# Kernel tuning notes

Hardware: AMD Instinct MI355X
Metric: run time of the kernel (lower is better)

Reference implementation:

```python
import jax, jax.numpy as jnp
import numpy as np

N = 50000; E = 800000; IN = 256; HID = 128; H = 4; C = 32; L = 3
REL = 100; RD = 16; EH = 32  # rel_emb_dim, edge-encoder hidden
LN_EPS = 1e-5


def _ln(x, g, b):
    m = jnp.mean(x, axis=-1, keepdims=True)
    v = jnp.mean((x - m) ** 2, axis=-1, keepdims=True)
    return (x - m) * jax.lax.rsqrt(v + LN_EPS) * g + b


def _mlp2(x, W1, b1, W2, b2):
    return jax.nn.relu(x @ W1 + b1) @ W2 + b2


def _forward(x, edge_attr, in_g, in_b, proj_W, proj_b,
             dist_W1, dist_b1, dist_W2, dist_b2,
             coexp_W1, coexp_b1, coexp_W2, coexp_b2,
             rel_emb, fus_W1, fus_b1, fus_ln_g, fus_ln_b, fus_W2, fus_b2,
             Wsrc, Wdst, Wedge, att, sscale, ng, nb, edge_index):
    src, dst = edge_index[0], edge_index[1]
    dist_w = edge_attr[:, 0]                              # [E] raw distance weight
    # ---- edge encoder ----
    dist_feat = _mlp2(edge_attr[:, 0:1], dist_W1, dist_b1, dist_W2, dist_b2)   # [E,RD]
    coexp_feat = _mlp2(edge_attr[:, 1:2], coexp_W1, coexp_b1, coexp_W2, coexp_b2)
    rel_id = jnp.clip(edge_attr[:, 2].astype(jnp.int32), 0, REL - 1)
    rel_feat = rel_emb[rel_id]                            # [E,RD]
    comb = jnp.concatenate([dist_feat, coexp_feat, rel_feat], axis=1)          # [E,3*RD]
    h = comb @ fus_W1 + fus_b1
    h = jax.nn.relu(_ln(h, fus_ln_g, fus_ln_b))
    edge_feat = h @ fus_W2 + fus_b2                       # [E,RD]
    # ---- input norm + projection ----
    x = _ln(x, in_g, in_b) @ proj_W + proj_b              # [N,HID]
    # ---- GAT layers ----
    for i in range(L):
        x_res = x
        xs = (x @ Wsrc[i]).reshape(N, H, C)
        xd = (x @ Wdst[i]).reshape(N, H, C)
        ef = (edge_feat @ Wedge[i]).reshape(E, H, C)
        a = jnp.tanh(xs[src] + xd[dst] + ef)              # [E,H,C]
        alpha = jnp.sum(a * att[i][None], axis=-1)        # [E,H]
        if i < L - 1:  # spatial_decay on all but last layer
            alpha = alpha * (dist_w[:, None] ** sscale[i][None, :])
        amax = jax.ops.segment_max(alpha, dst, num_segments=N)   # [N,H]
        ea = jnp.exp(alpha - amax[dst])
        esum = jax.ops.segment_sum(ea, dst, num_segments=N)
        alpha = ea / (esum[dst] + 1e-8)                   # [E,H]
        msg = xs[src] * alpha[..., None]                  # [E,H,C]
        out = jax.ops.segment_sum(msg, dst, num_segments=N).reshape(N, H * C)
        x = jax.nn.elu(_ln(out, ng[i], nb[i])) + x_res
    return x


def setup_inputs() -> dict:
    key = jax.random.key(0)
    ks = jax.random.split(key, 24)
    p = lambda k, s: jax.random.normal(k, s, jnp.float32) * 0.05
    edge_attr = jnp.concatenate([
        jax.random.uniform(ks[2], (E, 2), jnp.float32, 0.01, 1.0),
        jax.random.randint(ks[3], (E, 1), 0, REL).astype(jnp.float32)], axis=1)
    return dict(
        x=jax.random.normal(ks[0], (N, IN), jnp.float32),
        edge_index=jax.random.randint(ks[1], (2, E), 0, N),
        edge_attr=edge_attr,
        in_g=jnp.ones((IN,), jnp.float32), in_b=jnp.zeros((IN,), jnp.float32),
        proj_W=p(ks[4], (IN, HID)), proj_b=jnp.zeros((HID,), jnp.float32),
        dist_W1=p(ks[5], (1, EH)), dist_b1=jnp.zeros((EH,), jnp.float32),
        dist_W2=p(ks[6], (EH, RD)), dist_b2=jnp.zeros((RD,), jnp.float32),
        coexp_W1=p(ks[7], (1, EH)), coexp_b1=jnp.zeros((EH,), jnp.float32),
        coexp_W2=p(ks[8], (EH, RD)), coexp_b2=jnp.zeros((RD,), jnp.float32),
        rel_emb=p(ks[9], (REL, RD)),
        fus_W1=p(ks[10], (3 * RD, 2 * RD)), fus_b1=jnp.zeros((2 * RD,), jnp.float32),
        fus_ln_g=jnp.ones((2 * RD,), jnp.float32), fus_ln_b=jnp.zeros((2 * RD,), jnp.float32),
        fus_W2=p(ks[11], (2 * RD, RD)), fus_b2=jnp.zeros((RD,), jnp.float32),
        Wsrc=p(ks[12], (L, HID, HID)), Wdst=p(ks[13], (L, HID, HID)),
        Wedge=p(ks[14], (L, RD, HID)), att=p(ks[15], (L, H, C)),
        sscale=jnp.ones((L, H), jnp.float32),
        ng=jnp.ones((L, HID), jnp.float32), nb=jnp.zeros((L, HID), jnp.float32),
    )


def reference(x, edge_index, edge_attr, in_g, in_b, proj_W, proj_b,
              dist_W1, dist_b1, dist_W2, dist_b2,
              coexp_W1, coexp_b1, coexp_W2, coexp_b2,
              rel_emb, fus_W1, fus_b1, fus_ln_g, fus_ln_b, fus_W2, fus_b2,
              Wsrc, Wdst, Wedge, att, sscale, ng, nb):
    return _forward(x, edge_attr, in_g, in_b, proj_W, proj_b,
                    dist_W1, dist_b1, dist_W2, dist_b2,
                    coexp_W1, coexp_b1, coexp_W2, coexp_b2,
                    rel_emb, fus_W1, fus_b1, fus_ln_g, fus_ln_b, fus_W2, fus_b2,
                    Wsrc, Wdst, Wedge, att, sscale, ng, nb, edge_index)
```

## Files before the change

kernel.cpp:

```cpp
#include <hip/hip_runtime.h>
#include <math.h>

#define NN 50000
#define NE 800000
#define IND 256
#define HD 128
#define NH 4
#define NC 32
#define RELN 100
#define RD 16
#define EHD 32

typedef unsigned int uint;
typedef _Float16 half2_t __attribute__((ext_vector_type(2)));

__device__ inline uint pack_bf16(float a, float b) {
    uint ua = __float_as_uint(a), ub = __float_as_uint(b);
    ua += 0x7fffu + ((ua >> 16) & 1u);
    ub += 0x7fffu + ((ub >> 16) & 1u);
    return (ua >> 16) | (ub & 0xffff0000u);
}

__device__ inline uint pack_f16(float a, float b) {
    half2_t h = { (_Float16)a, (_Float16)b };
    return __builtin_bit_cast(uint, h);
}

#if __has_builtin(__builtin_amdgcn_fdot2)
#define FDOT2(a, b, c) __builtin_amdgcn_fdot2((a), (b), (c), false)
#else
static __device__ inline float FDOT2(half2_t a, half2_t b, float c) {
    return c + (float)a.x * (float)b.x + (float)a.y * (float)b.y;
}
#endif

__global__ __launch_bounds__(256) void count_kernel(
    const int* __restrict__ dst, int* __restrict__ counts)
{
    int e = blockIdx.x * 256 + threadIdx.x;
    if (e < NE) atomicAdd(&counts[dst[e]], 1);
}

__global__ __launch_bounds__(1024) void scan_kernel(
    const int* __restrict__ counts, int* __restrict__ row_ptr,
    int* __restrict__ cursor, int n)
{
    __shared__ int wsum[16];
    int tid = threadIdx.x;
    int C = (n + 1023) >> 10;
    int lo = tid * C, hi = min(lo + C, n);
    int s = 0;
    for (int i = lo; i < hi; i++) s += counts[i];
    int lane = tid & 63;
    int incl = s;
#pragma unroll
    for (int off = 1; off < 64; off <<= 1) {
        int v = __shfl_up(incl, off);
        if (lane >= off) incl += v;
    }
    if (lane == 63) wsum[tid >> 6] = incl;
    __syncthreads();
    if (tid < 16) {
        int v = wsum[tid];
        int inc2 = v;
#pragma unroll
        for (int off = 1; off < 16; off <<= 1) {
            int u = __shfl_up(inc2, off);
            if (tid >= off) inc2 += u;
        }
        wsum[tid] = inc2 - v;
    }
    __syncthreads();
    int run = wsum[tid >> 6] + (incl - s);
    for (int i = lo; i < hi; i++) {
        row_ptr[i] = run; cursor[i] = run; run += counts[i];
    }
    if (tid == 1023) row_ptr[n] = run;
}

__global__ __launch_bounds__(256) void edge_feat_fill_kernel(
    const float* __restrict__ eattr, const int* __restrict__ src,
    const int* __restrict__ dst, int* __restrict__ cursor,
    const float* __restrict__ dW1, const float* __restrict__ db1,
    const float* __restrict__ dW2, const float* __restrict__ db2,
    const float* __restrict__ cW1, const float* __restrict__ cb1,
    const float* __restrict__ cW2, const float* __restrict__ cb2,
    const float* __restrict__ rel_emb,
    const float* __restrict__ fW1, const float* __restrict__ fb1,
    const float* __restrict__ fg,  const float* __restrict__ fbl,
    const float* __restrict__ fW2, const float* __restrict__ fb2,
    uint4* __restrict__ efeat_h, int2* __restrict__ meta_c)
{
    int e = blockIdx.x * 256 + threadIdx.x;
    if (e >= NE) return;
    float d  = eattr[(size_t)e * 3 + 0];
    float cx = eattr[(size_t)e * 3 + 1];
    int r = (int)eattr[(size_t)e * 3 + 2];
    r = min(max(r, 0), RELN - 1);
    int p = atomicAdd(&cursor[dst[e]], 1);
    meta_c[p] = make_int2(src[e], __float_as_int(__log2f(d)));

    float df[RD], cf[RD];
#pragma unroll
    for (int k = 0; k < RD; k++) { df[k] = db2[k]; cf[k] = cb2[k]; }
    for (int j = 0; j < EHD; j++) {
        float h1 = fmaxf(d  * dW1[j] + db1[j], 0.f);
        float h2 = fmaxf(cx * cW1[j] + cb1[j], 0.f);
#pragma unroll
        for (int k = 0; k < RD; k++) {
            df[k] += h1 * dW2[j * RD + k];
            cf[k] += h2 * cW2[j * RD + k];
        }
    }
    float hh[2 * RD];
#pragma unroll
    for (int m = 0; m < 2 * RD; m++) hh[m] = fb1[m];
    for (int k = 0; k < RD; k++) {
        float a = df[k], b = cf[k], c = rel_emb[r * RD + k];
#pragma unroll
        for (int m = 0; m < 2 * RD; m++) {
            hh[m] += a * fW1[k * (2 * RD) + m]
                   + b * fW1[(RD + k) * (2 * RD) + m]
                   + c * fW1[(2 * RD + k) * (2 * RD) + m];
        }
    }
    float s = 0.f;
#pragma unroll
    for (int m = 0; m < 2 * RD; m++) s += hh[m];
    float mean = s * (1.f / (2 * RD));
    float s2 = 0.f;
#pragma unroll
    for (int m = 0; m < 2 * RD; m++) { float dd = hh[m] - mean; s2 += dd * dd; }
    float rs = rsqrtf(s2 * (1.f / (2 * RD)) + 1e-5f);
#pragma unroll
    for (int m = 0; m < 2 * RD; m++)
        hh[m] = fmaxf((hh[m] - mean) * rs * fg[m] + fbl[m], 0.f);

    float ef[RD];
#pragma unroll
    for (int k = 0; k < RD; k++) ef[k] = fb2[k];
    for (int m = 0; m < 2 * RD; m++) {
        float hv = hh[m];
#pragma unroll
        for (int k = 0; k < RD; k++) ef[k] += hv * fW2[m * RD + k];
    }
    uint4 e0, e1;
    e0.x = pack_f16(ef[0],  ef[1]);  e0.y = pack_f16(ef[2],  ef[3]);
    e0.z = pack_f16(ef[4],  ef[5]);  e0.w = pack_f16(ef[6],  ef[7]);
    e1.x = pack_f16(ef[8],  ef[9]);  e1.y = pack_f16(ef[10], ef[11]);
    e1.z = pack_f16(ef[12], ef[13]); e1.w = pack_f16(ef[14], ef[15]);
    efeat_h[(size_t)p * 2 + 0] = e0;
    efeat_h[(size_t)p * 2 + 1] = e1;
}

__global__ __launch_bounds__(256) void ln_proj_kernel(
    const float* __restrict__ x, const float* __restrict__ g, const float* __restrict__ b,
    const float* __restrict__ W, const float* __restrict__ pb, float* __restrict__ x0)
{
    __shared__ float xr[8][IND];
    __shared__ float mv[8][2];
    int nb = blockIdx.x * 8;
    int tid = threadIdx.x;
    const float4* xv = (const float4*)(x + (size_t)nb * IND);
    float4* xl = (float4*)&xr[0][0];
    xl[tid] = xv[tid];
    xl[tid + 256] = xv[tid + 256];
    __syncthreads();
    int node = tid >> 5, lane = tid & 31;
    float s1 = 0.f, s2 = 0.f;
#pragma unroll
    for (int j = 0; j < 8; j++) { float v = xr[node][lane + 32 * j]; s1 += v; s2 += v * v; }
#pragma unroll
    for (int off = 16; off >= 1; off >>= 1) { s1 += __shfl_xor(s1, off); s2 += __shfl_xor(s2, off); }
    if (lane == 0) {
        float mean = s1 * (1.f / IND);
        mv[node][0] = mean;
        mv[node][1] = rsqrtf(s2 * (1.f / IND) - mean * mean + 1e-5f);
    }
    __syncthreads();
#pragma unroll
    for (int j = 0; j < 8; j++) {
        int k = lane + 32 * j;
        xr[node][k] = (xr[node][k] - mv[node][0]) * mv[node][1] * g[k] + b[k];
    }
    __syncthreads();
    int col = tid & 127, r0 = (tid >> 7) * 4;
    float acc[4] = {0.f, 0.f, 0.f, 0.f};
    for (int k = 0; k < IND; k += 4) {
        float4 x4[4];
#pragma unroll
        for (int r = 0; r < 4; r++) x4[r] = *(const float4*)&xr[r0 + r][k];
        float w0 = W[(k + 0) * HD + col];
        float w1 = W[(k + 1) * HD + col];
        float w2 = W[(k + 2) * HD + col];
        float w3 = W[(k + 3) * HD + col];
#pragma unroll
        for (int r = 0; r < 4; r++)
            acc[r] += x4[r].x * w0 + x4[r].y * w1 + x4[r].z * w2 + x4[r].w * w3;
    }
    float pbv = pb[col];
#pragma unroll
    for (int r = 0; r < 4; r++)
        x0[(size_t)(nb + r0 + r) * HD + col] = acc[r] + pbv;
}

__global__ __launch_bounds__(512) void gemm_sd_kernel(
    const float* __restrict__ x, const float* __restrict__ Ws, const float* __restrict__ Wd,
    uint* __restrict__ xs_p, float2* __restrict__ xd2)
{
    __shared__ float xt[32][HD];
    int nb = blockIdx.x * 32;
    int tid = threadIdx.x;
    const float4* xv = (const float4*)(x + (size_t)nb * HD);
    float4* xl = (float4*)&xt[0][0];
    int validf4 = (NN - nb >= 32) ? 1024 : (NN - nb) * 32;
#pragma unroll
    for (int u = 0; u < 2; u++) {
        int idx = tid + u * 512;
        float4 v = {0.f, 0.f, 0.f, 0.f};
        if (idx < validf4) v = xv[idx];
        xl[idx] = v;
    }
    __syncthreads();
    int half = tid >> 8;
    int t = tid & 255;
    int q = t & 31;
    int r0 = (t >> 5) * 4;
    const float4* W4 = (const float4*)(half ? Wd : Ws);
    float4 acc[4] = { {0,0,0,0}, {0,0,0,0}, {0,0,0,0}, {0,0,0,0} };
    for (int k = 0; k < HD; k += 4) {
        float4 xr[4];
#pragma unroll
        for (int r = 0; r < 4; r++) xr[r] = *(const float4*)&xt[r0 + r][k];
        float4 w0 = W4[(k + 0) * 32 + q];
        float4 w1 = W4[(k + 1) * 32 + q];
        float4 w2 = W4[(k + 2) * 32 + q];
        float4 w3 = W4[(k + 3) * 32 + q];
#pragma unroll
        for (int r = 0; r < 4; r++) {
            acc[r].x += xr[r].x * w0.x + xr[r].y * w1.x + xr[r].z * w2.x + xr[r].w * w3.x;
            acc[r].y += xr[r].x * w0.y + xr[r].y * w1.y + xr[r].z * w2.y + xr[r].w * w3.y;
            acc[r].z += xr[r].x * w0.z + xr[r].y * w1.z + xr[r].z * w2.z + xr[r].w * w3.z;
            acc[r].w += xr[r].x * w0.w + xr[r].y * w1.w + xr[r].z * w2.w + xr[r].w * w3.w;
        }
    }
    if (half == 0) {
#pragma unroll
        for (int r = 0; r < 4; r++) {
            int n = nb + r0 + r;
            if (n < NN) {
                uint2 pk;
                pk.x = pack_bf16(acc[r].x, acc[r].y);
                pk.y = pack_bf16(acc[r].z, acc[r].w);
                *(uint2*)&xs_p[(size_t)n * 64 + 2 * q] = pk;
            }
        }
    } else {
#pragma unroll
        for (int r = 0; r < 4; r++) {
            int n = nb + r0 + r;
            if (n < NN) {
                float2* o = &xd2[(size_t)n * 64 + 2 * q];
                o[0] = make_float2(acc[r].x, acc[r].y);
                o[1] = make_float2(acc[r].z, acc[r].w);
            }
        }
    }
}

__global__ __launch_bounds__(256) void aggregate_kernel(
    const uint* __restrict__ xs_p, const float2* __restrict__ xd2,
    const uint4* __restrict__ efeat_h, const int2* __restrict__ meta_c,
    const int* __restrict__ row_ptr,
    const float* __restrict__ Wedge_i, const float2* __restrict__ att2,
    const float* __restrict__ sscale_i, const float2* __restrict__ ng2,
    const float2* __restrict__ nb2, float2* __restrict__ xio2,
    int apply_dist, int nwaves)
{
    int l = threadIdx.x & 63;
    int wid = blockIdx.x * 4 + __builtin_amdgcn_readfirstlane(threadIdx.x >> 6);

    int c0 = 2 * l, c1 = 2 * l + 1;
    half2_t wxh[8], wyh[8];
#pragma unroll
    for (int q = 0; q < 8; q++) {
        wxh[q] = (half2_t){ (_Float16)Wedge_i[(2 * q) * HD + c0],
                            (_Float16)Wedge_i[(2 * q + 1) * HD + c0] };
        wyh[q] = (half2_t){ (_Float16)Wedge_i[(2 * q) * HD + c1],
                            (_Float16)Wedge_i[(2 * q + 1) * HD + c1] };
    }
    float2 attv = att2[l];
    float sc = sscale_i[l >> 4];
    float2 g = ng2[l], bb = nb2[l];

    for (int node = wid; node < NN; node += nwaves) {
        int e0 = row_ptr[node], e1 = row_ptr[node + 1];
        float2 xdv  = xd2[(size_t)node * 64 + l];
        float2 xres = xio2[(size_t)node * 64 + l];
        float esum = 0.f;
        float2 macc = {0.f, 0.f};

        if (e0 < e1) {
            int2 mt[4]; uint xw[4]; uint4 ef[4][2];
#pragma unroll
            for (int j = 0; j < 4; j++) {
                int pp = min(e0 + j, e1 - 1);
                mt[j] = meta_c[pp];
                ef[j][0] = efeat_h[(size_t)pp * 2 + 0];
                ef[j][1] = efeat_h[(size_t)pp * 2 + 1];
            }
#pragma unroll
            for (int j = 0; j < 4; j++) xw[j] = xs_p[(size_t)mt[j].x * 64 + l];

#pragma unroll 2
            for (int b = e0; b < e1; b += 4) {
                int bn = b + 4;
                bool more = bn < e1;
                int2 mtn[4]; uint xwn[4]; uint4 efn[4][2];
                if (more) {
#pragma unroll
                    for (int j = 0; j < 4; j++) {
                        int pp = min(bn + j, e1 - 1);
                        mtn[j] = meta_c[pp];
                        efn[j][0] = efeat_h[(size_t)pp * 2 + 0];
                        efn[j][1] = efeat_h[(size_t)pp * 2 + 1];
                    }
#pragma unroll
                    for (int j = 0; j < 4; j++) xwn[j] = xs_p[(size_t)mtn[j].x * 64 + l];
                }
#pragma unroll
                for (int j = 0; j < 4; j++) {
                    const half2_t* eh = (const half2_t*)&ef[j][0];
                    float efx = 0.f, efy = 0.f;
#pragma unroll
                    for (int q = 0; q < 8; q++) {
                        efx = FDOT2(eh[q], wxh[q], efx);
                        efy = FDOT2(eh[q], wyh[q], efy);
                    }
                    float xvx = __uint_as_float(xw[j] << 16);
                    float xvy = __uint_as_float(xw[j] & 0xffff0000u);
                    float zx = xvx + xdv.x + efx;
                    float zy = xvy + xdv.y + efy;
                    float tx = 1.f - 2.f * __builtin_amdgcn_rcpf(__expf(2.f * zx) + 1.f);
                    float ty = 1.f - 2.f * __builtin_amdgcn_rcpf(__expf(2.f * zy) + 1.f);
                    float a = tx * attv.x + ty * attv.y;
#pragma unroll
                    for (int off = 8; off >= 1; off >>= 1) a += __shfl_xor(a, off);
                    if (apply_dist) a *= exp2f(__int_as_float(mt[j].y) * sc);
                    float ea = __expf(a);
                    ea = (b + j < e1) ? ea : 0.f;
                    esum += ea;
                    macc.x += xvx * ea;
                    macc.y += xvy * ea;
                }
                if (more) {
#pragma unroll
                    for (int j = 0; j < 4; j++) {
                        mt[j] = mtn[j]; xw[j] = xwn[j];
                        ef[j][0] = efn[j][0]; ef[j][1] = efn[j][1];
                    }
                }
            }
        }
        float inv = __builtin_amdgcn_rcpf(esum + 1e-8f);
        float2 outv = { macc.x * inv, macc.y * inv };

        float s1 = outv.x + outv.y;
        float s2 = outv.x * outv.x + outv.y * outv.y;
#pragma unroll
        for (int off = 32; off >= 1; off >>= 1) { s1 += __shfl_xor(s1, off); s2 += __shfl_xor(s2, off); }
        float mean = s1 * (1.f / HD);
        float var = s2 * (1.f / HD) - mean * mean;
        float rstd = rsqrtf(var + 1e-5f);
        float yx = (outv.x - mean) * rstd * g.x + bb.x;
        float yy = (outv.y - mean) * rstd * g.y + bb.y;
        float ex = (yx > 0.f) ? yx : expm1f(yx);
        float ey = (yy > 0.f) ? yy : expm1f(yy);
        float2 res;
        res.x = ex + xres.x;
        res.y = ey + xres.y;
        xio2[(size_t)node * 64 + l] = res;
    }
}

extern "C" void kernel_launch(void* const* d_in, const int* in_sizes, int n_in,
                              void* d_out, int out_size, void* d_ws, size_t ws_size,
                              hipStream_t stream)
{
    const float* x_in   = (const float*)d_in[0];
    const int*   eidx   = (const int*)  d_in[1];
    const float* eattr  = (const float*)d_in[2];
    const float* in_g   = (const float*)d_in[3];
    const float* in_b   = (const float*)d_in[4];
    const float* proj_W = (const float*)d_in[5];
    const float* proj_b = (const float*)d_in[6];
    const float* dW1    = (const float*)d_in[7];
    const float* db1    = (const float*)d_in[8];
    const float* dW2    = (const float*)d_in[9];
    const float* db2    = (const float*)d_in[10];
    const float* cW1    = (const float*)d_in[11];
    const float* cb1    = (const float*)d_in[12];
    const float* cW2    = (const float*)d_in[13];
    const float* cb2    = (const float*)d_in[14];
    const float* rel_emb= (const float*)d_in[15];
    const float* fW1    = (const float*)d_in[16];
    const float* fb1    = (const float*)d_in[17];
    const float* fg     = (const float*)d_in[18];
    const float* fbl    = (const float*)d_in[19];
    const float* fW2    = (const float*)d_in[20];
    const float* fb2    = (const float*)d_in[21];
    const float* Wsrc   = (const float*)d_in[22];
    const float* Wdst   = (const float*)d_in[23];
    const float* Wedge  = (const float*)d_in[24];
    const float* att    = (const float*)d_in[25];
    const float* sscale = (const float*)d_in[26];
    const float* ng     = (const float*)d_in[27];
    const float* nb     = (const float*)d_in[28];

    const int* src = eidx;
    const int* dst = eidx + NE;

    char* p = (char*)d_ws;
    auto alloc = [&](size_t bytes) -> void* {
        void* r = p;
        p += (bytes + 255) & ~(size_t)255;
        return r;
    };
    uint*  xs_p    = (uint*) alloc((size_t)NN * 64 * 4);
    float* xd      = (float*)alloc((size_t)NN * HD * 4);
    uint4* efeat_h = (uint4*)alloc((size_t)NE * 32);
    int*   counts  = (int*)  alloc((size_t)NN * 4);
    int*   row_ptr = (int*)  alloc(((size_t)NN + 1) * 4);
    int*   cursor  = (int*)  alloc((size_t)NN * 4);
    int2*  meta_c  = (int2*) alloc((size_t)NE * 8);

    float* x_cur = (float*)d_out;

    hipMemsetAsync(counts, 0, (size_t)NN * 4, stream);
    hipLaunchKernelGGL(count_kernel, dim3(NE / 256), dim3(256), 0, stream, dst, counts);
    hipLaunchKernelGGL(scan_kernel, dim3(1), dim3(1024), 0, stream,
        counts, row_ptr, cursor, NN);
    hipLaunchKernelGGL(edge_feat_fill_kernel, dim3(NE / 256), dim3(256), 0, stream,
        eattr, src, dst, cursor, dW1, db1, dW2, db2, cW1, cb1, cW2, cb2, rel_emb,
        fW1, fb1, fg, fbl, fW2, fb2, efeat_h, meta_c);
    hipLaunchKernelGGL(ln_proj_kernel, dim3(NN / 8), dim3(256), 0, stream,
        x_in, in_g, in_b, proj_W, proj_b, x_cur);

    const int AGG_BLOCKS = 2048;
    const int NWAVES = AGG_BLOCKS * 4;
    for (int i = 0; i < 3; i++) {
        hipLaunchKernelGGL(gemm_sd_kernel, dim3((NN + 31) / 32), dim3(512), 0, stream,
            x_cur, Wsrc + (size_t)i * HD * HD, Wdst + (size_t)i * HD * HD,
            xs_p, (float2*)xd);
        hipLaunchKernelGGL(aggregate_kernel, dim3(AGG_BLOCKS), dim3(256), 0, stream,
            xs_p, (const float2*)xd, efeat_h, meta_c, row_ptr,
            Wedge + (size_t)i * RD * HD, (const float2*)(att + (size_t)i * NH * NC),
            sscale + (size_t)i * NH,
            (const float2*)(ng + (size_t)i * HD), (const float2*)(nb + (size_t)i * HD),
            (float2*)x_cur, (i < 2) ? 1 : 0, NWAVES);
    }
}
```

Measured before the change: 942.2 us.

## Parallelize CSR scan, prefetch next node in aggregate, use DPP head reductions

Replaces the single-block serial prefix scan with a three-kernel multi-block scan. The aggregate kernel now prefetches the next node's edge batch and node data while finishing the current node, with sched_barriers to keep loads ahead of compute. The 16-lane shuffle reduction for attention logits becomes DPP row operations. These aim to cut serial scan latency, per-node pipeline bubbles and shuffle cost, at the price of more registers and two extra launches.

```diff
diff --git a/kernel.cpp b/kernel.cpp
--- a/kernel.cpp
+++ b/kernel.cpp
@@ -34,6 +34,24 @@
 }
 #endif
 
+__device__ inline float dpp_add(float a, const int ctrl) {
+    int t;
+    switch (ctrl) {
+        case 0: t = __builtin_amdgcn_update_dpp(0, __float_as_int(a), 0xB1,  0xF, 0xF, true); break;
+        case 1: t = __builtin_amdgcn_update_dpp(0, __float_as_int(a), 0x4E,  0xF, 0xF, true); break;
+        case 2: t = __builtin_amdgcn_update_dpp(0, __float_as_int(a), 0x141, 0xF, 0xF, true); break;
+        default:t = __builtin_amdgcn_update_dpp(0, __float_as_int(a), 0x140, 0xF, 0xF, true); break;
+    }
+    return a + __int_as_float(t);
+}
+__device__ inline float dpp_reduce16(float a) {
+    a = dpp_add(a, 0);
+    a = dpp_add(a, 1);
+    a = dpp_add(a, 2);
+    a = dpp_add(a, 3);
+    return a;
+}
+
 __global__ __launch_bounds__(256) void count_kernel(
     const int* __restrict__ dst, int* __restrict__ counts)
 {
@@ -41,41 +59,64 @@
     if (e < NE) atomicAdd(&counts[dst[e]], 1);
 }
 
-__global__ __launch_bounds__(1024) void scan_kernel(
+__global__ __launch_bounds__(1024) void scan_a_kernel(
     const int* __restrict__ counts, int* __restrict__ row_ptr,
-    int* __restrict__ cursor, int n)
+    int* __restrict__ partials, int n)
 {
     __shared__ int wsum[16];
     int tid = threadIdx.x;
-    int C = (n + 1023) >> 10;
-    int lo = tid * C, hi = min(lo + C, n);
-    int s = 0;
-    for (int i = lo; i < hi; i++) s += counts[i];
+    int i = blockIdx.x * 1024 + tid;
+    int v = (i < n) ? counts[i] : 0;
     int lane = tid & 63;
-    int incl = s;
+    int incl = v;
 #pragma unroll
     for (int off = 1; off < 64; off <<= 1) {
-        int v = __shfl_up(incl, off);
-        if (lane >= off) incl += v;
+        int t = __shfl_up(incl, off);
+        if (lane >= off) incl += t;
     }
     if (lane == 63) wsum[tid >> 6] = incl;
     __syncthreads();
     if (tid < 16) {
-        int v = wsum[tid];
-        int inc2 = v;
+        int w = wsum[tid];
+        int inc2 = w;
 #pragma unroll
         for (int off = 1; off < 16; off <<= 1) {
             int u = __shfl_up(inc2, off);
             if (tid >= off) inc2 += u;
         }
-        wsum[tid] = inc2 - v;
+        wsum[tid] = inc2 - w;
     }
     __syncthreads();
-    int run = wsum[tid >> 6] + (incl - s);
-    for (int i = lo; i < hi; i++) {
-        row_ptr[i] = run; cursor[i] = run; run += counts[i];
-    }
-    if (tid == 1023) row_ptr[n] = run;
+    int excl = wsum[tid >> 6] + incl - v;
+    if (i < n) row_ptr[i] = excl;
+    if (tid == 1023) partials[blockIdx.x] = excl + v;
+}
+
+__global__ __launch_bounds__(64) void scan_b_kernel(
+    int* __restrict__ partials, int* __restrict__ row_ptr, int nblk, int n)
+{
+    int tid = threadIdx.x;
+    int v = (tid < nblk) ? partials[tid] : 0;
+    int incl = v;
+#pragma unroll
+    for (int off = 1; off < 64; off <<= 1) {
+        int t = __shfl_up(incl, off);
+        if (tid >= off) incl += t;
+    }
+    if (tid < nblk) partials[tid] = incl - v;
+    if (tid == nblk - 1) row_ptr[n] = incl;
+}
+
+__global__ __launch_bounds__(1024) void scan_c_kernel(
+    int* __restrict__ row_ptr, int* __restrict__ cursor,
+    const int* __restrict__ partials, int n)
+{
+    int i = blockIdx.x * 1024 + threadIdx.x;
+    if (i < n) {
+        int r = row_ptr[i] + partials[blockIdx.x];
+        row_ptr[i] = r;
+        cursor[i] = r;
+    }
 }
 
 __global__ __launch_bounds__(256) void edge_feat_fill_kernel(
@@ -293,78 +334,50 @@
     float sc = sscale_i[l >> 4];
     float2 g = ng2[l], bb = nb2[l];
 
-    for (int node = wid; node < NN; node += nwaves) {
-        int e0 = row_ptr[node], e1 = row_ptr[node + 1];
-        float2 xdv  = xd2[(size_t)node * 64 + l];
-        float2 xres = xio2[(size_t)node * 64 + l];
-        float esum = 0.f;
-        float2 macc = {0.f, 0.f};
-
-        if (e0 < e1) {
-            int2 mt[4]; uint xw[4]; uint4 ef[4][2];
-#pragma unroll
-            for (int j = 0; j < 4; j++) {
-                int pp = min(e0 + j, e1 - 1);
-                mt[j] = meta_c[pp];
-                ef[j][0] = efeat_h[(size_t)pp * 2 + 0];
-                ef[j][1] = efeat_h[(size_t)pp * 2 + 1];
+    auto loadB = [&](int b, int e1, int2* mt, uint* xw, uint4 (*ef)[2]) {
+#pragma unroll
+        for (int j = 0; j < 4; j++) {
+            int pp = min(b + j, e1 - 1);
+            mt[j] = meta_c[pp];
+            ef[j][0] = efeat_h[(size_t)pp * 2 + 0];
+            ef[j][1] = efeat_h[(size_t)pp * 2 + 1];
+        }
+#pragma unroll
+        for (int j = 0; j < 4; j++) xw[j] = xs_p[(size_t)mt[j].x * 64 + l];
+    };
+
+    auto computeB = [&](int b, int e1, const int2* mt, const uint* xw,
+                        const uint4 (*ef)[2], float2 xdv,
+                        float& esum, float2& macc) {
+#pragma unroll
+        for (int j = 0; j < 4; j++) {
+            const half2_t* eh = (const half2_t*)&ef[j][0];
+            float efx = 0.f, efy = 0.f;
+#pragma unroll
+            for (int q = 0; q < 8; q++) {
+                efx = FDOT2(eh[q], wxh[q], efx);
+                efy = FDOT2(eh[q], wyh[q], efy);
             }
-#pragma unroll
-            for (int j = 0; j < 4; j++) xw[j] = xs_p[(size_t)mt[j].x * 64 + l];
-
-#pragma unroll 2
-            for (int b = e0; b < e1; b += 4) {
-                int bn = b + 4;
-                bool more = bn < e1;
-                int2 mtn[4]; uint xwn[4]; uint4 efn[4][2];
-                if (more) {
-#pragma unroll
-                    for (int j = 0; j < 4; j++) {
-                        int pp = min(bn + j, e1 - 1);
-                        mtn[j] = meta_c[pp];
-                        efn[j][0] = efeat_h[(size_t)pp * 2 + 0];
-                        efn[j][1] = efeat_h[(size_t)pp * 2 + 1];
-                    }
-#pragma unroll
-                    for (int j = 0; j < 4; j++) xwn[j] = xs_p[(size_t)mtn[j].x * 64 + l];
-                }
-#pragma unroll
-                for (int j = 0; j < 4; j++) {
-                    const half2_t* eh = (const half2_t*)&ef[j][0];
-                    float efx = 0.f, efy = 0.f;
-#pragma unroll
-                    for (int q = 0; q < 8; q++) {
-                        efx = FDOT2(eh[q], wxh[q], efx);
-                        efy = FDOT2(eh[q], wyh[q], efy);
-                    }
-                    float xvx = __uint_as_float(xw[j] << 16);
-                    float xvy = __uint_as_float(xw[j] & 0xffff0000u);
-                    float zx = xvx + xdv.x + efx;
-                    float zy = xvy + xdv.y + efy;
-                    float tx = 1.f - 2.f * __builtin_amdgcn_rcpf(__expf(2.f * zx) + 1.f);
-                    float ty = 1.f - 2.f * __builtin_amdgcn_rcpf(__expf(2.f * zy) + 1.f);
-                    float a = tx * attv.x + ty * attv.y;
-#pragma unroll
-                    for (int off = 8; off >= 1; off >>= 1) a += __shfl_xor(a, off);
-                    if (apply_dist) a *= exp2f(__int_as_float(mt[j].y) * sc);
-                    float ea = __expf(a);
-                    ea = (b + j < e1) ? ea : 0.f;
-                    esum += ea;
-                    macc.x += xvx * ea;
-                    macc.y += xvy * ea;
-                }
-                if (more) {
-#pragma unroll
-                    for (int j = 0; j < 4; j++) {
-                        mt[j] = mtn[j]; xw[j] = xwn[j];
-                        ef[j][0] = efn[j][0]; ef[j][1] = efn[j][1];
-                    }
-                }
-            }
-        }
+            float xvx = __uint_as_float(xw[j] << 16);
+            float xvy = __uint_as_float(xw[j] & 0xffff0000u);
+            float zx = xvx + xdv.x + efx;
+            float zy = xvy + xdv.y + efy;
+            float tx = 1.f - 2.f * __builtin_amdgcn_rcpf(__expf(2.f * zx) + 1.f);
+            float ty = 1.f - 2.f * __builtin_amdgcn_rcpf(__expf(2.f * zy) + 1.f);
+            float a = tx * attv.x + ty * attv.y;
+            a = dpp_reduce16(a);
+            if (apply_dist) a *= exp2f(__int_as_float(mt[j].y) * sc);
+            float ea = __expf(a);
+            ea = (b + j < e1) ? ea : 0.f;
+            esum += ea;
+            macc.x += xvx * ea;
+            macc.y += xvy * ea;
+        }
+    };
+
+    auto epilogue = [&](int node, float esum, float2 macc, float2 xres) {
         float inv = __builtin_amdgcn_rcpf(esum + 1e-8f);
         float2 outv = { macc.x * inv, macc.y * inv };
-
         float s1 = outv.x + outv.y;
         float s2 = outv.x * outv.x + outv.y * outv.y;
 #pragma unroll
@@ -380,6 +393,53 @@
         res.x = ex + xres.x;
         res.y = ey + xres.y;
         xio2[(size_t)node * 64 + l] = res;
+    };
+
+    int node = wid;
+    if (node >= NN) return;
+    int e0 = row_ptr[node], e1 = row_ptr[node + 1];
+    float2 xdv  = xd2[(size_t)node * 64 + l];
+    float2 xres = xio2[(size_t)node * 64 + l];
+    int2 mt[4], mtn[4];
+    uint xw[4], xwn[4];
+    uint4 ef[4][2], efn[4][2];
+    if (e0 < e1) loadB(e0, e1, mt, xw, ef);
+    float esum = 0.f;
+    float2 macc = {0.f, 0.f};
+
+    while (true) {
+        int b = e0;
+#pragma unroll 2
+        for (; b + 4 < e1; b += 4) {
+            loadB(b + 4, e1, mtn, xwn, efn);
+            __builtin_amdgcn_sched_barrier(0);
+            computeB(b, e1, mt, xw, ef, xdv, esum, macc);
+#pragma unroll
+            for (int j = 0; j < 4; j++) {
+                mt[j] = mtn[j]; xw[j] = xwn[j];
+                ef[j][0] = efn[j][0]; ef[j][1] = efn[j][1];
+            }
+        }
+        int nnode = node + nwaves;
+        int ne0 = 0, ne1 = 0;
+        float2 nxdv = {0.f, 0.f}, nxres = {0.f, 0.f};
+        if (nnode < NN) {
+            ne0 = row_ptr[nnode]; ne1 = row_ptr[nnode + 1];
+            nxdv  = xd2[(size_t)nnode * 64 + l];
+            nxres = xio2[(size_t)nnode * 64 + l];
+            if (ne0 < ne1) loadB(ne0, ne1, mtn, xwn, efn);
+        }
+        __builtin_amdgcn_sched_barrier(0);
+        if (b < e1) computeB(b, e1, mt, xw, ef, xdv, esum, macc);
+        epilogue(node, esum, macc, xres);
+        if (nnode >= NN) break;
+        node = nnode; e0 = ne0; e1 = ne1; xdv = nxdv; xres = nxres;
+        esum = 0.f; macc = make_float2(0.f, 0.f);
+#pragma unroll
+        for (int j = 0; j < 4; j++) {
+            mt[j] = mtn[j]; xw[j] = xwn[j];
+            ef[j][0] = efn[j][0]; ef[j][1] = efn[j][1];
+        }
     }
 }
 
@@ -433,13 +493,20 @@
     int*   row_ptr = (int*)  alloc(((size_t)NN + 1) * 4);
     int*   cursor  = (int*)  alloc((size_t)NN * 4);
     int2*  meta_c  = (int2*) alloc((size_t)NE * 8);
+    int*   partials= (int*)  alloc(256);
 
     float* x_cur = (float*)d_out;
+
+    const int SCAN_NBLK = (NN + 1023) / 1024;
 
     hipMemsetAsync(counts, 0, (size_t)NN * 4, stream);
     hipLaunchKernelGGL(count_kernel, dim3(NE / 256), dim3(256), 0, stream, dst, counts);
-    hipLaunchKernelGGL(scan_kernel, dim3(1), dim3(1024), 0, stream,
-        counts, row_ptr, cursor, NN);
+    hipLaunchKernelGGL(scan_a_kernel, dim3(SCAN_NBLK), dim3(1024), 0, stream,
+        counts, row_ptr, partials, NN);
+    hipLaunchKernelGGL(scan_b_kernel, dim3(1), dim3(64), 0, stream,
+        partials, row_ptr, SCAN_NBLK, NN);
+    hipLaunchKernelGGL(scan_c_kernel, dim3(SCAN_NBLK), dim3(1024), 0, stream,
+        row_ptr, cursor, partials, NN);
     hipLaunchKernelGGL(edge_feat_fill_kernel, dim3(NE / 256), dim3(256), 0, stream,
         eattr, src, dst, cursor, dW1, db1, dW2, db2, cW1, cb1, cW2, cb2, rel_emb,
         fW1, fb1, fg, fbl, fW2, fb2, efeat_h, meta_c);
```

Result: faster. 781.1 us (-17.1%).
